# Performance work log

Measured on AMD Instinct MI355X. Metric: run time of the kernel, lower is better.

Reference implementation:

```python
import jax, jax.numpy as jnp
import numpy as np

MAX_ONSET_DELAY_SAMPLES = 10


def apply_delays(templates, delays):
    # templates: (E, F, L), delays: (E, F) -> shifted templates with zero fill
    E, F, L = templates.shape
    d = jnp.round(jnp.clip(delays, -MAX_ONSET_DELAY_SAMPLES, MAX_ONSET_DELAY_SAMPLES)).astype(jnp.int32)
    idx = jnp.arange(L)                                   # (L,)
    src = idx[None, None, :] - d[:, :, None]              # (E, F, L) source index for torch.roll(shift=d)
    valid = (src >= 0) & (src < L)                        # zero out wrapped-around region
    src_c = jnp.clip(src, 0, L - 1)
    shifted = jnp.take_along_axis(templates, src_c, axis=2)
    return jnp.where(valid, shifted, jnp.zeros((), templates.dtype))


def setup_inputs() -> dict:
    key = jax.random.key(0)
    k1, k2, k3 = jax.random.split(key, 3)
    B, S, F = 64, 32768, 6
    E, L = 16, 80
    x = jax.random.normal(k1, (B, S, F), dtype=jnp.float32)
    templates = jax.random.normal(k2, (E, F, L), dtype=jnp.float32) * 0.1
    onset_delays = jax.random.normal(k3, (E, F), dtype=jnp.float32)
    return {"x": x, "templates": templates, "onset_delays": onset_delays}


def reference(x, templates, onset_delays):
    # x: (B, S, F); templates: (E, F, L); onset_delays: (E, F) -> scores (B, S, E)
    B, S, F = x.shape
    E, _, L = templates.shape
    delayed = apply_delays(templates, onset_delays)       # (E, F, L)
    kern = jnp.flip(delayed, axis=2)                      # torch flips template before conv1d
    pad = (L - 1) // 2
    # Fuse the 96 per-(event,feature) conv1d calls into one conv: sum over features
    # is exactly the input-channel contraction of a dense conv1d (in=F, out=E).
    score = jax.lax.conv_general_dilated(
        jnp.transpose(x, (0, 2, 1)),                      # (B, F, S)
        kern,                                             # (E, F, L) as OIH
        window_strides=(1,),
        padding=[(pad, pad)],
        dimension_numbers=("NCH", "OIH", "NCH"),
    )                                                     # (B, E, S_out)
    S_out = score.shape[2]
    if S_out > S:
        score = score[:, :, :S]
    elif S_out < S:
        score = jnp.pad(score, ((0, 0), (0, 0), (0, S - S_out)))
    return jnp.transpose(score, (0, 2, 1)) / (L * F)      # (B, S, E)
```

## Files before the change

### kernel.cpp

```cpp
#include <hip/hip_runtime.h>

#define BB 64
#define SS 32768
#define FF 6
#define EE 16
#define LL 80
#define KK 480
#define NSL 15
#define TBLK 128
#define NPHI 8
#define WROW 208
#define WLDST 488

typedef _Float16 half8 __attribute__((ext_vector_type(8)));
typedef float f32x4 __attribute__((ext_vector_type(4)));

struct __align__(4) hpair { _Float16 a, b; };

__global__ void prep_kernel(const float* __restrict__ tpl, const float* __restrict__ dly,
                            _Float16* __restrict__ wrev) {
    int n = blockIdx.x * 256 + threadIdx.x;
    if (n >= EE * KK) return;
    int e = n / KK, k = n - e * KK;
    int f = k / LL, r = k - f * LL;
    int m = LL - 1 - r;
    float dl = fminf(fmaxf(dly[e * FF + f], -10.f), 10.f);
    int d = (int)rintf(dl);
    int src = m - d;
    float v = (src >= 0 && src < LL) ? tpl[(e * FF + f) * LL + src] : 0.f;
    wrev[n] = (_Float16)v;
}

template <bool FROM_WS>
__global__ __launch_bounds__(512, 4) void corr_kernel(
    const float* __restrict__ x, const float* __restrict__ tpl,
    const float* __restrict__ dly, const _Float16* __restrict__ wrev,
    float* __restrict__ out) {
    __shared__ alignas(16) _Float16 Wlds[EE * WLDST];
    __shared__ alignas(16) _Float16 xs[NPHI][FF][WROW];

    int tid = threadIdx.x;
    int b = blockIdx.x >> 8;
    int t0 = (blockIdx.x & 255) << 7;

    if (FROM_WS) {
        for (int gi = tid; gi < EE * KK / 8; gi += 512) {
            int e = gi / 60;
            int k8 = (gi - e * 60) * 8;
            *(uint4*)&Wlds[e * WLDST + k8] = *(const uint4*)&wrev[e * KK + k8];
        }
    } else {
        for (int n = tid; n < EE * KK; n += 512) {
            int e = n / KK, k = n - e * KK;
            int f = k / LL, r = k - f * LL;
            int m = LL - 1 - r;
            float dl = fminf(fmaxf(dly[e * FF + f], -10.f), 10.f);
            int d = (int)rintf(dl);
            int src = m - d;
            float v = (src >= 0 && src < LL) ? tpl[(e * FF + f) * LL + src] : 0.f;
            Wlds[e * WLDST + k] = (_Float16)v;
        }
    }

    const float* xb = x + (size_t)b * (SS * FF);
    for (int it = tid; it < NPHI * 100; it += 512) {
        int phi = it / 100;
        int i = (it - phi * 100) * 2;
        int pos = t0 + phi - 39 + i;
        float va[12];
        if (pos >= 0 && pos <= SS - 2) {
            const float* xp = xb + (size_t)pos * FF;
            #pragma unroll
            for (int q = 0; q < 6; q++)
                *(float2*)&va[2 * q] = *(const float2*)&xp[2 * q];
        } else {
            #pragma unroll
            for (int q = 0; q < 2; q++) {
                int p = pos + q;
                bool ok = (p >= 0) && (p < SS);
                #pragma unroll
                for (int f = 0; f < FF; f++)
                    va[q * 6 + f] = ok ? xb[(size_t)p * FF + f] : 0.f;
            }
        }
        #pragma unroll
        for (int f = 0; f < FF; f++) {
            hpair hp;
            hp.a = (_Float16)va[f];
            hp.b = (_Float16)va[6 + f];
            *(hpair*)&xs[phi][f][i] = hp;
        }
    }
    __syncthreads();

    int lane = tid & 63;
    int wid = tid >> 6;
    int e = lane & 15;
    int g = lane >> 4;

    half8 bq[NSL];
    #pragma unroll
    for (int s = 0; s < NSL; s++)
        bq[s] = *(const half8*)&Wlds[e * WLDST + 32 * s + 8 * g];

    int phi = wid;
    f32x4 acc = {0.f, 0.f, 0.f, 0.f};
    int row16 = 8 * (lane & 15);
    #pragma unroll
    for (int s = 0; s < NSL; s++) {
        int k0 = 32 * s + 8 * g;
        int f = (k0 * 205) >> 14;
        int r0 = k0 - 80 * f;
        const half8 a = *(const half8*)&xs[phi][f][row16 + r0];
        acc = __builtin_amdgcn_mfma_f32_16x16x32_f16(a, bq[s], acc, 0, 0, 0);
    }

    #pragma unroll
    for (int j = 0; j < 4; j++) {
        int row = g * 4 + j;
        int t = t0 + phi + 8 * row;
        float v = acc[j] * (1.0f / 480.0f);
        if (t == SS - 1) v = 0.f;
        out[((size_t)b * SS + t) * EE + e] = v;
    }
}

extern "C" void kernel_launch(void* const* d_in, const int* in_sizes, int n_in,
                              void* d_out, int out_size, void* d_ws, size_t ws_size,
                              hipStream_t stream) {
    const float* x = (const float*)d_in[0];
    const float* tpl = (const float*)d_in[1];
    const float* dly = (const float*)d_in[2];
    float* out = (float*)d_out;

    int grid = BB * (SS / TBLK);
    if (ws_size >= (size_t)(EE * KK * sizeof(_Float16))) {
        _Float16* wrev = (_Float16*)d_ws;
        prep_kernel<<<(EE * KK + 255) / 256, 256, 0, stream>>>(tpl, dly, wrev);
        corr_kernel<true><<<grid, 512, 0, stream>>>(x, tpl, dly, wrev, out);
    } else {
        corr_kernel<false><<<grid, 512, 0, stream>>>(x, tpl, dly, nullptr, out);
    }
}
```

Baseline: 77.82 us.

## Double time tile per block and reuse staged weights across two MFMA tiles

Each block now covers 256 time steps using 4 phases instead of 8. Each wave computes two 16-row MFMA tiles, so the weight registers are reused and the per-block weight staging and launch overhead are amortised over more output. The halo overhead of the x staging shrinks, and the fp16 packing now uses the cvt_pkrtz builtin. The A-operand LDS reads are split into 8-byte loads because the row stride is now 4 halves. This may add LDS bank conflicts and instructions, and pkrtz rounds toward zero instead of to nearest.

Result: faster. 66.98 us (-13.9%).

```diff
diff --git a/kernel.cpp b/kernel.cpp
--- a/kernel.cpp
+++ b/kernel.cpp
@@ -7,15 +7,15 @@
 #define LL 80
 #define KK 480
 #define NSL 15
-#define TBLK 128
-#define NPHI 8
-#define WROW 208
+#define TBLK 256
+#define NPHI 4
+#define ROWS 64
+#define WROW 336
+#define WUNITS 166
 #define WLDST 488
 
 typedef _Float16 half8 __attribute__((ext_vector_type(8)));
 typedef float f32x4 __attribute__((ext_vector_type(4)));
-
-struct __align__(4) hpair { _Float16 a, b; };
 
 __global__ void prep_kernel(const float* __restrict__ tpl, const float* __restrict__ dly,
                             _Float16* __restrict__ wrev) {
@@ -40,8 +40,8 @@
     __shared__ alignas(16) _Float16 xs[NPHI][FF][WROW];
 
     int tid = threadIdx.x;
-    int b = blockIdx.x >> 8;
-    int t0 = (blockIdx.x & 255) << 7;
+    int b = blockIdx.x >> 7;
+    int t0 = (blockIdx.x & 127) << 8;
 
     if (FROM_WS) {
         for (int gi = tid; gi < EE * KK / 8; gi += 512) {
@@ -63,9 +63,9 @@
     }
 
     const float* xb = x + (size_t)b * (SS * FF);
-    for (int it = tid; it < NPHI * 100; it += 512) {
-        int phi = it / 100;
-        int i = (it - phi * 100) * 2;
+    for (int it = tid; it < NPHI * WUNITS; it += 512) {
+        int phi = it / WUNITS;
+        int i = (it - phi * WUNITS) * 2;
         int pos = t0 + phi - 39 + i;
         float va[12];
         if (pos >= 0 && pos <= SS - 2) {
@@ -85,10 +85,14 @@
         }
         #pragma unroll
         for (int f = 0; f < FF; f++) {
-            hpair hp;
-            hp.a = (_Float16)va[f];
-            hp.b = (_Float16)va[6 + f];
-            *(hpair*)&xs[phi][f][i] = hp;
+#if __has_builtin(__builtin_amdgcn_cvt_pkrtz)
+            __fp16 __attribute__((ext_vector_type(2))) hp =
+                __builtin_amdgcn_cvt_pkrtz(va[f], va[6 + f]);
+            *(decltype(hp)*)&xs[phi][f][i] = hp;
+#else
+            xs[phi][f][i] = (_Float16)va[f];
+            xs[phi][f][i + 1] = (_Float16)va[6 + f];
+#endif
         }
     }
     __syncthreads();
@@ -97,31 +101,46 @@
     int wid = tid >> 6;
     int e = lane & 15;
     int g = lane >> 4;
+    int phi = wid & 3;
+    int pairi = wid >> 2;
 
     half8 bq[NSL];
     #pragma unroll
     for (int s = 0; s < NSL; s++)
         bq[s] = *(const half8*)&Wlds[e * WLDST + 32 * s + 8 * g];
 
-    int phi = wid;
-    f32x4 acc = {0.f, 0.f, 0.f, 0.f};
-    int row16 = 8 * (lane & 15);
+    const char* xph = (const char*)&xs[phi][0][0];
+    f32x4 acc[2];
     #pragma unroll
-    for (int s = 0; s < NSL; s++) {
-        int k0 = 32 * s + 8 * g;
-        int f = (k0 * 205) >> 14;
-        int r0 = k0 - 80 * f;
-        const half8 a = *(const half8*)&xs[phi][f][row16 + r0];
-        acc = __builtin_amdgcn_mfma_f32_16x16x32_f16(a, bq[s], acc, 0, 0, 0);
+    for (int tt = 0; tt < 2; tt++) acc[tt] = (f32x4){0.f, 0.f, 0.f, 0.f};
+
+    #pragma unroll
+    for (int tt = 0; tt < 2; tt++) {
+        int R = pairi * 32 + tt * 16 + (lane & 15);
+        #pragma unroll
+        for (int s = 0; s < NSL; s++) {
+            int k0 = 32 * s + 8 * g;
+            int f = (k0 * 205) >> 14;
+            int r0 = k0 - 80 * f;
+            const char* p = xph + 2 * (f * WROW + 4 * R + r0);
+            uint2 lo = *(const uint2*)p;
+            uint2 hi = *(const uint2*)(p + 8);
+            union { unsigned u[4]; half8 h; } av;
+            av.u[0] = lo.x; av.u[1] = lo.y; av.u[2] = hi.x; av.u[3] = hi.y;
+            acc[tt] = __builtin_amdgcn_mfma_f32_16x16x32_f16(av.h, bq[s], acc[tt], 0, 0, 0);
+        }
     }
 
     #pragma unroll
-    for (int j = 0; j < 4; j++) {
-        int row = g * 4 + j;
-        int t = t0 + phi + 8 * row;
-        float v = acc[j] * (1.0f / 480.0f);
-        if (t == SS - 1) v = 0.f;
-        out[((size_t)b * SS + t) * EE + e] = v;
+    for (int tt = 0; tt < 2; tt++) {
+        #pragma unroll
+        for (int j = 0; j < 4; j++) {
+            int row = pairi * 32 + tt * 16 + g * 4 + j;
+            int t = t0 + phi + 4 * row;
+            float v = acc[tt][j] * (1.0f / 480.0f);
+            if (t == SS - 1) v = 0.f;
+            out[((size_t)b * SS + t) * EE + e] = v;
+        }
     }
 }
 
```
